# Kernel optimization log

Measured on AMD Instinct MI355X. Metric: run time of the kernel, lower is better.

## Reference

```python
import jax, jax.numpy as jnp
import numpy as np

N = 50000
E = 800000
IN_CH = 128
HID = 16
HEADS = 8
OUT_CH = 64
NEG_SLOPE = 0.2


def setup_inputs() -> dict:
    key = jax.random.key(0)
    ks = jax.random.split(key, 16)
    x = jax.random.normal(ks[0], (N, IN_CH), dtype=jnp.float32)
    edge_index = jax.random.randint(ks[1], (2, E), 0, N, dtype=jnp.int64)
    s = 0.05
    # GATv2 layer 1: in=128 -> heads=8, out=16 (concat -> 128)
    W1l = jax.random.normal(ks[2], (IN_CH, HEADS * HID), dtype=jnp.float32) * s
    b1l = jnp.zeros((HEADS * HID,), dtype=jnp.float32)
    W1r = jax.random.normal(ks[3], (IN_CH, HEADS * HID), dtype=jnp.float32) * s
    b1r = jnp.zeros((HEADS * HID,), dtype=jnp.float32)
    att1 = jax.random.normal(ks[4], (HEADS, HID), dtype=jnp.float32) * s
    bias1 = jnp.zeros((HEADS * HID,), dtype=jnp.float32)
    # GATv2 layer 2: in=128 -> heads=1, out=64
    W2l = jax.random.normal(ks[5], (HEADS * HID, OUT_CH), dtype=jnp.float32) * s
    b2l = jnp.zeros((OUT_CH,), dtype=jnp.float32)
    W2r = jax.random.normal(ks[6], (HEADS * HID, OUT_CH), dtype=jnp.float32) * s
    b2r = jnp.zeros((OUT_CH,), dtype=jnp.float32)
    att2 = jax.random.normal(ks[7], (1, OUT_CH), dtype=jnp.float32) * s
    bias2 = jnp.zeros((OUT_CH,), dtype=jnp.float32)
    return dict(x=x, edge_index=edge_index,
                W1l=W1l, b1l=b1l, W1r=W1r, b1r=b1r, att1=att1, bias1=bias1,
                W2l=W2l, b2l=b2l, W2r=W2r, b2r=b2r, att2=att2, bias2=bias2)


def gatv2_conv(x, src, dst, Wl, bl, Wr, br, att, bias, heads, out_ch, concat):
    n = x.shape[0]
    xl = (x @ Wl + bl).reshape(n, heads, out_ch)  # source transform
    xr = (x @ Wr + br).reshape(n, heads, out_ch)  # target transform
    m = xl[src] + xr[dst]                          # [E, H, C]
    m = jnp.where(m > 0, m, NEG_SLOPE * m)         # LeakyReLU(0.2)
    alpha = jnp.einsum('ehc,hc->eh', m, att)       # [E, H]
    # segment softmax over destination nodes (every node has a self loop)
    amax = jax.ops.segment_max(alpha, dst, num_segments=n)
    ea = jnp.exp(alpha - amax[dst])
    denom = jax.ops.segment_sum(ea, dst, num_segments=n)
    w = ea / denom[dst]                            # [E, H]
    out = jax.ops.segment_sum(xl[src] * w[:, :, None], dst, num_segments=n)
    if concat:
        out = out.reshape(n, heads * out_ch)
    else:
        out = out.mean(axis=1)
    return out + bias


def reference(x, edge_index, W1l, b1l, W1r, b1r, att1, bias1,
              W2l, b2l, W2r, b2r, att2, bias2):
    n = x.shape[0]
    loops = jnp.arange(n, dtype=edge_index.dtype)
    src = jnp.concatenate([edge_index[0], loops])
    dst = jnp.concatenate([edge_index[1], loops])
    # dropout layers are identity in eval mode
    h = gatv2_conv(x, src, dst, W1l, b1l, W1r, b1r, att1, bias1,
                   heads=HEADS, out_ch=HID, concat=True)
    h = jax.nn.elu(h)
    out = gatv2_conv(h, src, dst, W2l, b2l, W2r, b2r, att2, bias2,
                     heads=1, out_ch=OUT_CH, concat=True)
    return out
```

## Files before the change

### kernel.cpp

```cpp
#include <hip/hip_runtime.h>
#include <hip/hip_bf16.h>

constexpr int N_  = 50000;
constexpr int E_  = 800000;
constexpr int ET_ = 850000;
constexpr float NEG_SLOPE = 0.2f;

constexpr int SCAN_NB = (N_ + 255) / 256;
constexpr int CSR_CAP = 1250008;
constexpr int HT      = ET_ / 8;
constexpr int HB      = (HT + 255) / 256;
constexpr int G1B     = N_ / 16;
constexpr int ZERO4   = (50000 + CSR_CAP) / 4;

typedef __attribute__((ext_vector_type(8))) short short8;
typedef __attribute__((ext_vector_type(4))) float f32x4;

__device__ inline float leaky(float v) { return fmaxf(v, NEG_SLOPE * v); }

__device__ inline unsigned bf16rn(float f) {
    union { float f; unsigned u; } v; v.f = f;
    return (v.u + 0x7fffu + ((v.u >> 16) & 1u)) >> 16;
}
__device__ inline float2 unpack2(unsigned u) {
    return make_float2(__uint_as_float(u << 16), __uint_as_float(u & 0xffff0000u));
}

__global__ __launch_bounds__(256) void init_kernel(
        const float* __restrict__ W1l, const float* __restrict__ W1r,
        const float* __restrict__ W2l, const float* __restrict__ W2r,
        unsigned short* __restrict__ wsw, unsigned short* __restrict__ wsw2,
        int4* __restrict__ zbase) {
    int gid = blockIdx.x * 256 + threadIdx.x;
    if (gid < ZERO4) zbase[gid] = make_int4(0, 0, 0, 0);
    if (gid < 32768) {
        int j    = gid & 7;
        int lane = (gid >> 3) & 63;
        int ks   = (gid >> 9) & 3;
        int ct   = gid >> 11;
        int k = ks * 32 + ((lane >> 4) & 3) * 8 + j;
        int c = ct * 16 + (lane & 15);
        float v = (c < 128) ? W1l[k * 128 + c] : W1r[k * 128 + (c - 128)];
        wsw[gid] = (unsigned short)bf16rn(v);
    } else if (gid < 49152) {
        int t2   = gid - 32768;
        int j    = t2 & 7;
        int lane = (t2 >> 3) & 63;
        int ks   = (t2 >> 9) & 3;
        int ct   = t2 >> 11;
        int k = ks * 32 + ((lane >> 4) & 3) * 8 + j;
        int c = ct * 16 + (lane & 15);
        float v = (c < 64) ? W2l[k * 64 + c] : W2r[k * 64 + (c - 64)];
        wsw2[t2] = (unsigned short)bf16rn(v);
    }
}

__global__ __launch_bounds__(256) void hist_kernel(
        const int* __restrict__ ei, int* __restrict__ count) {
    int t = blockIdx.x * 256 + threadIdx.x;
    if (t >= HT) return;
    int e8 = t * 8;
    int d[8];
    if (e8 < E_) {
        int4 a = *(const int4*)(ei + E_ + e8);
        int4 b = *(const int4*)(ei + E_ + e8 + 4);
        d[0] = a.x; d[1] = a.y; d[2] = a.z; d[3] = a.w;
        d[4] = b.x; d[5] = b.y; d[6] = b.z; d[7] = b.w;
    } else {
        #pragma unroll
        for (int i = 0; i < 8; ++i) d[i] = e8 + i - E_;
    }
    #pragma unroll
    for (int i = 0; i < 8; ++i) atomicAdd(&count[d[i]], 1);
}

__global__ __launch_bounds__(256) void scan_partial(
        const int* __restrict__ count, int* __restrict__ bsum) {
    __shared__ int red[256];
    int t = threadIdx.x;
    int i = blockIdx.x * 256 + t;
    red[t] = (i < N_) ? ((count[i] + 7) & ~7) : 0;
    __syncthreads();
    #pragma unroll
    for (int o = 128; o > 0; o >>= 1) {
        if (t < o) red[t] += red[t + o];
        __syncthreads();
    }
    if (t == 0) bsum[blockIdx.x] = red[0];
}

__global__ __launch_bounds__(256) void scan_final2(
        const int* __restrict__ count, const int* __restrict__ bsum,
        int* __restrict__ start, int* __restrict__ cur) {
    __shared__ int top[256];
    __shared__ int buf[256];
    int t = threadIdx.x;
    top[t] = (t < SCAN_NB) ? bsum[t] : 0;
    __syncthreads();
    #pragma unroll
    for (int o = 1; o < 256; o <<= 1) {
        int add = (t >= o) ? top[t - o] : 0;
        __syncthreads();
        top[t] += add;
        __syncthreads();
    }
    int bst = (blockIdx.x == 0) ? 0 : top[blockIdx.x - 1];
    int i = blockIdx.x * 256 + t;
    int v = (i < N_) ? ((count[i] + 7) & ~7) : 0;
    buf[t] = v;
    __syncthreads();
    #pragma unroll
    for (int o = 1; o < 256; o <<= 1) {
        int add = (t >= o) ? buf[t - o] : 0;
        __syncthreads();
        buf[t] += add;
        __syncthreads();
    }
    if (i < N_) {
        int sv = bst + buf[t] - v;
        start[i] = sv;
        cur[i]   = sv;
    }
}

__global__ __launch_bounds__(256) void scatter_gemm1(
        const int* __restrict__ ei, int* __restrict__ cur,
        int* __restrict__ csr_src,
        const float* __restrict__ x, const unsigned short* __restrict__ wsw,
        const float* __restrict__ bl, const float* __restrict__ br,
        unsigned short* __restrict__ xlu, float* __restrict__ xr1) {
    __shared__ unsigned short lu[16][132];
    __shared__ float          lr[16][132];
    if (blockIdx.x < HB) {
        int t = blockIdx.x * 256 + threadIdx.x;
        if (t >= HT) return;
        int e8 = t * 8;
        int s[8], d[8];
        if (e8 < E_) {
            int4 sa = *(const int4*)(ei + e8);
            int4 sb = *(const int4*)(ei + e8 + 4);
            int4 da = *(const int4*)(ei + E_ + e8);
            int4 db = *(const int4*)(ei + E_ + e8 + 4);
            s[0] = sa.x; s[1] = sa.y; s[2] = sa.z; s[3] = sa.w;
            s[4] = sb.x; s[5] = sb.y; s[6] = sb.z; s[7] = sb.w;
            d[0] = da.x; d[1] = da.y; d[2] = da.z; d[3] = da.w;
            d[4] = db.x; d[5] = db.y; d[6] = db.z; d[7] = db.w;
        } else {
            #pragma unroll
            for (int i = 0; i < 8; ++i) { s[i] = e8 + i - E_; d[i] = s[i]; }
        }
        int o[8];
        #pragma unroll
        for (int i = 0; i < 8; ++i) o[i] = atomicAdd(&cur[d[i]], 1);
        #pragma unroll
        for (int i = 0; i < 8; ++i) csr_src[o[i]] = s[i];
        return;
    }
    const int blk  = blockIdx.x - HB;
    const int wave = threadIdx.x >> 6;
    const int lane = threadIdx.x & 63;
    const int n0 = blk * 16;
    const int m = lane & 15;
    const int q = (lane >> 4) & 3;
    const float* __restrict__ arow = x + (size_t)(n0 + m) * 128 + q * 8;
    short8 afrag[4];
    #pragma unroll
    for (int ks = 0; ks < 4; ++ks) {
        float4 v0 = *(const float4*)(arow + ks * 32);
        float4 v1 = *(const float4*)(arow + ks * 32 + 4);
        short8 a;
        a[0] = (short)bf16rn(v0.x); a[1] = (short)bf16rn(v0.y);
        a[2] = (short)bf16rn(v0.z); a[3] = (short)bf16rn(v0.w);
        a[4] = (short)bf16rn(v1.x); a[5] = (short)bf16rn(v1.y);
        a[6] = (short)bf16rn(v1.z); a[7] = (short)bf16rn(v1.w);
        afrag[ks] = a;
    }
    #pragma unroll
    for (int i = 0; i < 4; ++i) {
        const int ct = wave * 4 + i;
        f32x4 acc = {0.f, 0.f, 0.f, 0.f};
        #pragma unroll
        for (int ks = 0; ks < 4; ++ks) {
            short8 b = *(const short8*)(wsw + ((size_t)(ct * 4 + ks) * 64 + lane) * 8);
            acc = __builtin_amdgcn_mfma_f32_16x16x32_bf16(afrag[ks], b, acc, 0, 0, 0);
        }
        if (ct < 8) {
            const int col = ct * 16 + m;
            float bias = bl[col];
            #pragma unroll
            for (int j = 0; j < 4; ++j)
                lu[q * 4 + j][col] = (unsigned short)bf16rn(acc[j] + bias);
        } else {
            const int col = (ct - 8) * 16 + m;
            float bias = br[col];
            #pragma unroll
            for (int j = 0; j < 4; ++j)
                lr[q * 4 + j][col] = acc[j] + bias;
        }
    }
    __syncthreads();
    unsigned* __restrict__ xlu32 = (unsigned*)xlu;
    #pragma unroll
    for (int k = 0; k < 4; ++k) {
        int r = wave * 4 + k;
        unsigned w = *(const unsigned*)&lu[r][2 * lane];
        xlu32[(size_t)(n0 + r) * 64 + lane] = w;
        float2 f = make_float2(lr[r][2 * lane], lr[r][2 * lane + 1]);
        *(float2*)(xr1 + (size_t)(n0 + r) * 128 + 2 * lane) = f;
    }
}

__global__ __launch_bounds__(256) void fused1(
        const int* __restrict__ csr_src, const int* __restrict__ start,
        const int* __restrict__ count,
        const unsigned* __restrict__ xl1b, const float* __restrict__ xr1,
        const float* __restrict__ att, const float* __restrict__ bias1,
        float* __restrict__ hout) {
    int t = blockIdx.x * 256 + threadIdx.x;
    int n = __builtin_amdgcn_readfirstlane(t >> 6);
    int lane = t & 63;
    if (n >= N_) return;
    float2 xr = *(const float2*)(xr1 + (size_t)n * 128 + 2 * lane);
    float2 av = *(const float2*)(att + 2 * lane);
    int p0 = __builtin_amdgcn_readfirstlane(start[n]);
    int p1 = p0 + __builtin_amdgcn_readfirstlane(count[n]);
    float2 acc = make_float2(0.f, 0.f);
    float l = 0.f;
    for (int p = p0; p < p1; p += 4) {
        int4 si = *(const int4*)(csr_src + p);
        int s0 = __builtin_amdgcn_readfirstlane(si.x);
        int s1 = __builtin_amdgcn_readfirstlane(si.y);
        int s2 = __builtin_amdgcn_readfirstlane(si.z);
        int s3 = __builtin_amdgcn_readfirstlane(si.w);
        float2 x0 = unpack2(xl1b[(size_t)s0 * 64 + lane]);
        float2 x1 = unpack2(xl1b[(size_t)s1 * 64 + lane]);
        float2 x2 = unpack2(xl1b[(size_t)s2 * 64 + lane]);
        float2 x3 = unpack2(xl1b[(size_t)s3 * 64 + lane]);
        float a0 = fmaf(leaky(x0.x + xr.x), av.x, leaky(x0.y + xr.y) * av.y);
        float a1 = fmaf(leaky(x1.x + xr.x), av.x, leaky(x1.y + xr.y) * av.y);
        float a2 = fmaf(leaky(x2.x + xr.x), av.x, leaky(x2.y + xr.y) * av.y);
        float a3 = fmaf(leaky(x3.x + xr.x), av.x, leaky(x3.y + xr.y) * av.y);
        a0 += __shfl_xor(a0, 1); a1 += __shfl_xor(a1, 1);
        a2 += __shfl_xor(a2, 1); a3 += __shfl_xor(a3, 1);
        a0 += __shfl_xor(a0, 2); a1 += __shfl_xor(a1, 2);
        a2 += __shfl_xor(a2, 2); a3 += __shfl_xor(a3, 2);
        a0 += __shfl_xor(a0, 4); a1 += __shfl_xor(a1, 4);
        a2 += __shfl_xor(a2, 4); a3 += __shfl_xor(a3, 4);
        float w0 = __expf(a0);
        float w1 = p + 1 < p1 ? __expf(a1) : 0.f;
        float w2 = p + 2 < p1 ? __expf(a2) : 0.f;
        float w3 = p + 3 < p1 ? __expf(a3) : 0.f;
        acc.x = fmaf(w0, x0.x, acc.x); acc.y = fmaf(w0, x0.y, acc.y); l += w0;
        acc.x = fmaf(w1, x1.x, acc.x); acc.y = fmaf(w1, x1.y, acc.y); l += w1;
        acc.x = fmaf(w2, x2.x, acc.x); acc.y = fmaf(w2, x2.y, acc.y); l += w2;
        acc.x = fmaf(w3, x3.x, acc.x); acc.y = fmaf(w3, x3.y, acc.y); l += w3;
    }
    float2 bv = *(const float2*)(bias1 + 2 * lane);
    float vx = acc.x / l + bv.x;
    float vy = acc.y / l + bv.y;
    float2 o;
    o.x = vx > 0.f ? vx : (__expf(vx) - 1.f);
    o.y = vy > 0.f ? vy : (__expf(vy) - 1.f);
    *(float2*)(hout + (size_t)n * 128 + 2 * lane) = o;
}

__global__ __launch_bounds__(256) void gemm2_mfma(
        const float* __restrict__ hbuf,
        const unsigned short* __restrict__ wsw2,
        const float* __restrict__ bl, const float* __restrict__ br,
        unsigned short* __restrict__ xlu2, float* __restrict__ xr2) {
    __shared__ unsigned short lu2[16][68];
    __shared__ float          lr2[16][68];
    const int wave = threadIdx.x >> 6;
    const int lane = threadIdx.x & 63;
    const int n0 = blockIdx.x * 16;
    const int m = lane & 15;
    const int q = (lane >> 4) & 3;
    const float* __restrict__ arow = hbuf + (size_t)(n0 + m) * 128 + q * 8;
    short8 afrag[4];
    #pragma unroll
    for (int ks = 0; ks < 4; ++ks) {
        float4 v0 = *(const float4*)(arow + ks * 32);
        float4 v1 = *(const float4*)(arow + ks * 32 + 4);
        short8 a;
        a[0] = (short)bf16rn(v0.x); a[1] = (short)bf16rn(v0.y);
        a[2] = (short)bf16rn(v0.z); a[3] = (short)bf16rn(v0.w);
        a[4] = (short)bf16rn(v1.x); a[5] = (short)bf16rn(v1.y);
        a[6] = (short)bf16rn(v1.z); a[7] = (short)bf16rn(v1.w);
        afrag[ks] = a;
    }
    #pragma unroll
    for (int i = 0; i < 2; ++i) {
        const int ct = wave * 2 + i;
        f32x4 acc = {0.f, 0.f, 0.f, 0.f};
        #pragma unroll
        for (int ks = 0; ks < 4; ++ks) {
            short8 b = *(const short8*)(wsw2 + ((size_t)(ct * 4 + ks) * 64 + lane) * 8);
            acc = __builtin_amdgcn_mfma_f32_16x16x32_bf16(afrag[ks], b, acc, 0, 0, 0);
        }
        if (ct < 4) {
            const int col = ct * 16 + m;
            float bias = bl[col];
            #pragma unroll
            for (int j = 0; j < 4; ++j)
                lu2[q * 4 + j][col] = (unsigned short)bf16rn(acc[j] + bias);
        } else {
            const int col = (ct - 4) * 16 + m;
            float bias = br[col];
            #pragma unroll
            for (int j = 0; j < 4; ++j)
                lr2[q * 4 + j][col] = acc[j] + bias;
        }
    }
    __syncthreads();
    unsigned* __restrict__ xlu232 = (unsigned*)xlu2;
    #pragma unroll
    for (int k = 0; k < 2; ++k) {
        int rr = wave * 4 + 2 * k + (lane >> 5);
        int c  = lane & 31;
        unsigned w = *(const unsigned*)&lu2[rr][2 * c];
        xlu232[(size_t)(n0 + rr) * 32 + c] = w;
    }
    #pragma unroll
    for (int k = 0; k < 4; ++k) {
        int r = wave * 4 + k;
        xr2[(size_t)(n0 + r) * 64 + lane] = lr2[r][lane];
    }
}

__global__ __launch_bounds__(256) void fused2(
        const int* __restrict__ csr_src, const int* __restrict__ start,
        const int* __restrict__ count,
        const unsigned* __restrict__ xl2b, const float* __restrict__ xr2,
        const float* __restrict__ att, const float* __restrict__ bias2,
        float* __restrict__ out) {
    int t = blockIdx.x * 256 + threadIdx.x;
    int n = __builtin_amdgcn_readfirstlane(t >> 6);
    int lane = t & 63;
    int half = lane >> 5;
    int lc   = lane & 31;
    if (n >= N_) return;
    float2 xr = *(const float2*)(xr2 + (size_t)n * 64 + 2 * lc);
    float2 av = *(const float2*)(att + 2 * lc);
    int p0 = __builtin_amdgcn_readfirstlane(start[n]);
    int p1 = p0 + __builtin_amdgcn_readfirstlane(count[n]);
    float2 acc = make_float2(0.f, 0.f);
    float l = 0.f;
    for (int p = p0; p < p1; p += 8) {
        int4 ia = *(const int4*)(csr_src + p);
        int4 ib = *(const int4*)(csr_src + p + 4);
        int sx[8];
        sx[0] = __builtin_amdgcn_readfirstlane(ia.x);
        sx[1] = __builtin_amdgcn_readfirstlane(ia.y);
        sx[2] = __builtin_amdgcn_readfirstlane(ia.z);
        sx[3] = __builtin_amdgcn_readfirstlane(ia.w);
        sx[4] = __builtin_amdgcn_readfirstlane(ib.x);
        sx[5] = __builtin_amdgcn_readfirstlane(ib.y);
        sx[6] = __builtin_amdgcn_readfirstlane(ib.z);
        sx[7] = __builtin_amdgcn_readfirstlane(ib.w);
        #pragma unroll
        for (int u = 0; u < 4; ++u) {
            int pe = p + 2 * u + half;
            int s  = sx[2 * u + half];
            float2 xv = unpack2(xl2b[(size_t)s * 32 + lc]);
            float a = fmaf(leaky(xv.x + xr.x), av.x, leaky(xv.y + xr.y) * av.y);
            a += __shfl_xor(a, 1);
            a += __shfl_xor(a, 2);
            a += __shfl_xor(a, 4);
            a += __shfl_xor(a, 8);
            a += __shfl_xor(a, 16);
            float w = pe < p1 ? __expf(a) : 0.f;
            acc.x = fmaf(w, xv.x, acc.x);
            acc.y = fmaf(w, xv.y, acc.y);
            l += w;
        }
    }
    acc.x += __shfl_xor(acc.x, 32);
    acc.y += __shfl_xor(acc.y, 32);
    l     += __shfl_xor(l, 32);
    if (half == 0) {
        float2 bv = *(const float2*)(bias2 + 2 * lc);
        float2 o;
        o.x = acc.x / l + bv.x;
        o.y = acc.y / l + bv.y;
        *(float2*)(out + (size_t)n * 64 + 2 * lc) = o;
    }
}

extern "C" void kernel_launch(void* const* d_in, const int* in_sizes, int n_in,
                              void* d_out, int out_size, void* d_ws, size_t ws_size,
                              hipStream_t stream) {
    (void)in_sizes; (void)n_in; (void)out_size; (void)ws_size;
    const float* x     = (const float*)d_in[0];
    const int*   ei    = (const int*)d_in[1];
    const float* W1l   = (const float*)d_in[2];
    const float* b1l   = (const float*)d_in[3];
    const float* W1r   = (const float*)d_in[4];
    const float* b1r   = (const float*)d_in[5];
    const float* att1  = (const float*)d_in[6];
    const float* bias1 = (const float*)d_in[7];
    const float* W2l   = (const float*)d_in[8];
    const float* b2l   = (const float*)d_in[9];
    const float* W2r   = (const float*)d_in[10];
    const float* b2r   = (const float*)d_in[11];
    const float* att2  = (const float*)d_in[12];
    const float* bias2 = (const float*)d_in[13];
    float* out = (float*)d_out;

    float* xr1      = (float*)d_ws;
    float* hbuf     = xr1 + 6400000;
    unsigned* xl1b  = (unsigned*)(hbuf + 6400000);
    int* count   = (int*)(xl1b + 3200000);
    int* csr_src = count + 50000;
    int* startp  = csr_src + CSR_CAP;
    int* cur     = startp + 50000;
    int* bsum    = cur + 850000;
    int* bstart  = bsum + 256;
    unsigned short* wsw2 = (unsigned short*)(bstart + 256);
    unsigned* xl2b = xl1b;
    float* xr2     = xr1;
    unsigned short* wsw = (unsigned short*)hbuf;

    init_kernel<<<(ZERO4 + 255) / 256, 256, 0, stream>>>(W1l, W1r, W2l, W2r,
                                                         wsw, wsw2, (int4*)count);
    hist_kernel<<<HB, 256, 0, stream>>>(ei, count);
    scan_partial<<<SCAN_NB, 256, 0, stream>>>(count, bsum);
    scan_final2 <<<SCAN_NB, 256, 0, stream>>>(count, bsum, startp, cur);
    scatter_gemm1<<<HB + G1B, 256, 0, stream>>>(ei, cur, csr_src, x, wsw,
                                                b1l, b1r,
                                                (unsigned short*)xl1b, xr1);
    fused1<<<(N_ * 64 + 255) / 256, 256, 0, stream>>>(csr_src, startp, count,
                                                      xl1b, xr1, att1, bias1, hbuf);
    gemm2_mfma <<<N_ / 16, 256, 0, stream>>>(hbuf, wsw2, b2l, b2r,
                                             (unsigned short*)xl2b, xr2);
    fused2<<<(N_ * 64 + 255) / 256, 256, 0, stream>>>(csr_src, startp, count,
                                                      xl2b, xr2, att2, bias2, out);
}
```

Baseline: 293.9 us.

## Split GEMM1 across histogram and scatter launches; unroll fused1 edge loop to 8

The standalone histogram kernel is merged into a two-phase edge/GEMM kernel. Half of the layer-1 GEMM tiles run alongside the degree histogram and the other half alongside the CSR scatter, so the atomic-heavy edge work overlaps dense MFMA work in both launches. Separately, the layer-1 aggregation loop now processes 8 CSR neighbours per iteration instead of 4, giving more gathers in flight. This relies on CSR segments being padded to multiples of 8, which the scan already does, and raises register pressure in fused1.

```diff
diff --git a/kernel.cpp b/kernel.cpp
--- a/kernel.cpp
+++ b/kernel.cpp
@@ -10,7 +10,8 @@
 constexpr int CSR_CAP = 1250008;
 constexpr int HT      = ET_ / 8;
 constexpr int HB      = (HT + 255) / 256;
-constexpr int G1B     = N_ / 16;
+constexpr int G1A     = 1563;
+constexpr int G1Bb    = 1562;
 constexpr int ZERO4   = (50000 + CSR_CAP) / 4;
 
 typedef __attribute__((ext_vector_type(8))) short short8;
@@ -55,25 +56,6 @@
     }
 }
 
-__global__ __launch_bounds__(256) void hist_kernel(
-        const int* __restrict__ ei, int* __restrict__ count) {
-    int t = blockIdx.x * 256 + threadIdx.x;
-    if (t >= HT) return;
-    int e8 = t * 8;
-    int d[8];
-    if (e8 < E_) {
-        int4 a = *(const int4*)(ei + E_ + e8);
-        int4 b = *(const int4*)(ei + E_ + e8 + 4);
-        d[0] = a.x; d[1] = a.y; d[2] = a.z; d[3] = a.w;
-        d[4] = b.x; d[5] = b.y; d[6] = b.z; d[7] = b.w;
-    } else {
-        #pragma unroll
-        for (int i = 0; i < 8; ++i) d[i] = e8 + i - E_;
-    }
-    #pragma unroll
-    for (int i = 0; i < 8; ++i) atomicAdd(&count[d[i]], 1);
-}
-
 __global__ __launch_bounds__(256) void scan_partial(
         const int* __restrict__ count, int* __restrict__ bsum) {
     __shared__ int red[256];
@@ -123,9 +105,10 @@
     }
 }
 
-__global__ __launch_bounds__(256) void scatter_gemm1(
-        const int* __restrict__ ei, int* __restrict__ cur,
-        int* __restrict__ csr_src,
+__global__ __launch_bounds__(256) void edge_gemm1(
+        const int phase, const int nbase,
+        const int* __restrict__ ei, int* __restrict__ count,
+        int* __restrict__ cur, int* __restrict__ csr_src,
         const float* __restrict__ x, const unsigned short* __restrict__ wsw,
         const float* __restrict__ bl, const float* __restrict__ br,
         unsigned short* __restrict__ xlu, float* __restrict__ xr1) {
@@ -135,31 +118,46 @@
         int t = blockIdx.x * 256 + threadIdx.x;
         if (t >= HT) return;
         int e8 = t * 8;
-        int s[8], d[8];
-        if (e8 < E_) {
-            int4 sa = *(const int4*)(ei + e8);
-            int4 sb = *(const int4*)(ei + e8 + 4);
-            int4 da = *(const int4*)(ei + E_ + e8);
-            int4 db = *(const int4*)(ei + E_ + e8 + 4);
-            s[0] = sa.x; s[1] = sa.y; s[2] = sa.z; s[3] = sa.w;
-            s[4] = sb.x; s[5] = sb.y; s[6] = sb.z; s[7] = sb.w;
-            d[0] = da.x; d[1] = da.y; d[2] = da.z; d[3] = da.w;
-            d[4] = db.x; d[5] = db.y; d[6] = db.z; d[7] = db.w;
+        if (phase == 0) {
+            int d[8];
+            if (e8 < E_) {
+                int4 a = *(const int4*)(ei + E_ + e8);
+                int4 b = *(const int4*)(ei + E_ + e8 + 4);
+                d[0] = a.x; d[1] = a.y; d[2] = a.z; d[3] = a.w;
+                d[4] = b.x; d[5] = b.y; d[6] = b.z; d[7] = b.w;
+            } else {
+                #pragma unroll
+                for (int i = 0; i < 8; ++i) d[i] = e8 + i - E_;
+            }
+            #pragma unroll
+            for (int i = 0; i < 8; ++i) atomicAdd(&count[d[i]], 1);
         } else {
-            #pragma unroll
-            for (int i = 0; i < 8; ++i) { s[i] = e8 + i - E_; d[i] = s[i]; }
-        }
-        int o[8];
-        #pragma unroll
-        for (int i = 0; i < 8; ++i) o[i] = atomicAdd(&cur[d[i]], 1);
-        #pragma unroll
-        for (int i = 0; i < 8; ++i) csr_src[o[i]] = s[i];
+            int s[8], d[8];
+            if (e8 < E_) {
+                int4 sa = *(const int4*)(ei + e8);
+                int4 sb = *(const int4*)(ei + e8 + 4);
+                int4 da = *(const int4*)(ei + E_ + e8);
+                int4 db = *(const int4*)(ei + E_ + e8 + 4);
+                s[0] = sa.x; s[1] = sa.y; s[2] = sa.z; s[3] = sa.w;
+                s[4] = sb.x; s[5] = sb.y; s[6] = sb.z; s[7] = sb.w;
+                d[0] = da.x; d[1] = da.y; d[2] = da.z; d[3] = da.w;
+                d[4] = db.x; d[5] = db.y; d[6] = db.z; d[7] = db.w;
+            } else {
+                #pragma unroll
+                for (int i = 0; i < 8; ++i) { s[i] = e8 + i - E_; d[i] = s[i]; }
+            }
+            int o[8];
+            #pragma unroll
+            for (int i = 0; i < 8; ++i) o[i] = atomicAdd(&cur[d[i]], 1);
+            #pragma unroll
+            for (int i = 0; i < 8; ++i) csr_src[o[i]] = s[i];
+        }
         return;
     }
     const int blk  = blockIdx.x - HB;
     const int wave = threadIdx.x >> 6;
     const int lane = threadIdx.x & 63;
-    const int n0 = blk * 16;
+    const int n0 = nbase + blk * 16;
     const int m = lane & 15;
     const int q = (lane >> 4) & 3;
     const float* __restrict__ arow = x + (size_t)(n0 + m) * 128 + q * 8;
@@ -226,34 +224,61 @@
     int p1 = p0 + __builtin_amdgcn_readfirstlane(count[n]);
     float2 acc = make_float2(0.f, 0.f);
     float l = 0.f;
-    for (int p = p0; p < p1; p += 4) {
-        int4 si = *(const int4*)(csr_src + p);
-        int s0 = __builtin_amdgcn_readfirstlane(si.x);
-        int s1 = __builtin_amdgcn_readfirstlane(si.y);
-        int s2 = __builtin_amdgcn_readfirstlane(si.z);
-        int s3 = __builtin_amdgcn_readfirstlane(si.w);
+    for (int p = p0; p < p1; p += 8) {
+        int4 ia = *(const int4*)(csr_src + p);
+        int4 ib = *(const int4*)(csr_src + p + 4);
+        int s0 = __builtin_amdgcn_readfirstlane(ia.x);
+        int s1 = __builtin_amdgcn_readfirstlane(ia.y);
+        int s2 = __builtin_amdgcn_readfirstlane(ia.z);
+        int s3 = __builtin_amdgcn_readfirstlane(ia.w);
+        int s4 = __builtin_amdgcn_readfirstlane(ib.x);
+        int s5 = __builtin_amdgcn_readfirstlane(ib.y);
+        int s6 = __builtin_amdgcn_readfirstlane(ib.z);
+        int s7 = __builtin_amdgcn_readfirstlane(ib.w);
         float2 x0 = unpack2(xl1b[(size_t)s0 * 64 + lane]);
         float2 x1 = unpack2(xl1b[(size_t)s1 * 64 + lane]);
         float2 x2 = unpack2(xl1b[(size_t)s2 * 64 + lane]);
         float2 x3 = unpack2(xl1b[(size_t)s3 * 64 + lane]);
+        float2 x4 = unpack2(xl1b[(size_t)s4 * 64 + lane]);
+        float2 x5 = unpack2(xl1b[(size_t)s5 * 64 + lane]);
+        float2 x6 = unpack2(xl1b[(size_t)s6 * 64 + lane]);
+        float2 x7 = unpack2(xl1b[(size_t)s7 * 64 + lane]);
         float a0 = fmaf(leaky(x0.x + xr.x), av.x, leaky(x0.y + xr.y) * av.y);
         float a1 = fmaf(leaky(x1.x + xr.x), av.x, leaky(x1.y + xr.y) * av.y);
         float a2 = fmaf(leaky(x2.x + xr.x), av.x, leaky(x2.y + xr.y) * av.y);
         float a3 = fmaf(leaky(x3.x + xr.x), av.x, leaky(x3.y + xr.y) * av.y);
+        float a4 = fmaf(leaky(x4.x + xr.x), av.x, leaky(x4.y + xr.y) * av.y);
+        float a5 = fmaf(leaky(x5.x + xr.x), av.x, leaky(x5.y + xr.y) * av.y);
+        float a6 = fmaf(leaky(x6.x + xr.x), av.x, leaky(x6.y + xr.y) * av.y);
+        float a7 = fmaf(leaky(x7.x + xr.x), av.x, leaky(x7.y + xr.y) * av.y);
         a0 += __shfl_xor(a0, 1); a1 += __shfl_xor(a1, 1);
         a2 += __shfl_xor(a2, 1); a3 += __shfl_xor(a3, 1);
+        a4 += __shfl_xor(a4, 1); a5 += __shfl_xor(a5, 1);
+        a6 += __shfl_xor(a6, 1); a7 += __shfl_xor(a7, 1);
         a0 += __shfl_xor(a0, 2); a1 += __shfl_xor(a1, 2);
         a2 += __shfl_xor(a2, 2); a3 += __shfl_xor(a3, 2);
+        a4 += __shfl_xor(a4, 2); a5 += __shfl_xor(a5, 2);
+        a6 += __shfl_xor(a6, 2); a7 += __shfl_xor(a7, 2);
         a0 += __shfl_xor(a0, 4); a1 += __shfl_xor(a1, 4);
         a2 += __shfl_xor(a2, 4); a3 += __shfl_xor(a3, 4);
+        a4 += __shfl_xor(a4, 4); a5 += __shfl_xor(a5, 4);
+        a6 += __shfl_xor(a6, 4); a7 += __shfl_xor(a7, 4);
         float w0 = __expf(a0);
         float w1 = p + 1 < p1 ? __expf(a1) : 0.f;
         float w2 = p + 2 < p1 ? __expf(a2) : 0.f;
         float w3 = p + 3 < p1 ? __expf(a3) : 0.f;
+        float w4 = p + 4 < p1 ? __expf(a4) : 0.f;
+        float w5 = p + 5 < p1 ? __expf(a5) : 0.f;
+        float w6 = p + 6 < p1 ? __expf(a6) : 0.f;
+        float w7 = p + 7 < p1 ? __expf(a7) : 0.f;
         acc.x = fmaf(w0, x0.x, acc.x); acc.y = fmaf(w0, x0.y, acc.y); l += w0;
         acc.x = fmaf(w1, x1.x, acc.x); acc.y = fmaf(w1, x1.y, acc.y); l += w1;
         acc.x = fmaf(w2, x2.x, acc.x); acc.y = fmaf(w2, x2.y, acc.y); l += w2;
         acc.x = fmaf(w3, x3.x, acc.x); acc.y = fmaf(w3, x3.y, acc.y); l += w3;
+        acc.x = fmaf(w4, x4.x, acc.x); acc.y = fmaf(w4, x4.y, acc.y); l += w4;
+        acc.x = fmaf(w5, x5.x, acc.x); acc.y = fmaf(w5, x5.y, acc.y); l += w5;
+        acc.x = fmaf(w6, x6.x, acc.x); acc.y = fmaf(w6, x6.y, acc.y); l += w6;
+        acc.x = fmaf(w7, x7.x, acc.x); acc.y = fmaf(w7, x7.y, acc.y); l += w7;
     }
     float2 bv = *(const float2*)(bias1 + 2 * lane);
     float vx = acc.x / l + bv.x;
@@ -423,12 +448,14 @@
 
     init_kernel<<<(ZERO4 + 255) / 256, 256, 0, stream>>>(W1l, W1r, W2l, W2r,
                                                          wsw, wsw2, (int4*)count);
-    hist_kernel<<<HB, 256, 0, stream>>>(ei, count);
+    edge_gemm1<<<HB + G1A, 256, 0, stream>>>(0, 0, ei, count, cur, csr_src,
+                                             x, wsw, b1l, b1r,
+                                             (unsigned short*)xl1b, xr1);
     scan_partial<<<SCAN_NB, 256, 0, stream>>>(count, bsum);
     scan_final2 <<<SCAN_NB, 256, 0, stream>>>(count, bsum, startp, cur);
-    scatter_gemm1<<<HB + G1B, 256, 0, stream>>>(ei, cur, csr_src, x, wsw,
-                                                b1l, b1r,
-                                                (unsigned short*)xl1b, xr1);
+    edge_gemm1<<<HB + G1Bb, 256, 0, stream>>>(1, G1A * 16, ei, count, cur, csr_src,
+                                              x, wsw, b1l, b1r,
+                                              (unsigned short*)xl1b, xr1);
     fused1<<<(N_ * 64 + 255) / 256, 256, 0, stream>>>(csr_src, startp, count,
                                                       xl1b, xr1, att1, bias1, hbuf);
     gemm2_mfma <<<N_ / 16, 256, 0, stream>>>(hbuf, wsw2, b2l, b2r,
```

After: 296.7 us. About the same (+0.9%).
